# Optimization experiments

Measured on AMD Instinct MI355X. Metric: run time of the kernel, lower is better.

The kernel has to match this reference:

```python
import jax, jax.numpy as jnp
import numpy as np

B, H, P, D, NF = 16, 16, 128, 128, 12  # patches == head_dim required by lin_qk


def setup_inputs() -> dict:
    key = jax.random.key(0)
    ks = jax.random.split(key, 8)
    return {
        "q": jax.random.normal(ks[0], (B, H, P, D), jnp.float32),
        "k": jax.random.normal(ks[1], (B, H, P, D), jnp.float32),
        "scale": jnp.ones((1,), jnp.float32),  # unused by the original forward
        "grid": jnp.arange(NF, dtype=jnp.float32) + 1.0,
        "base_weight": jax.random.uniform(ks[2], (D, D), jnp.float32),
        "coef_q": jax.random.uniform(ks[3], (D, NF), jnp.float32),
        "coef_k": jax.random.uniform(ks[4], (D, NF), jnp.float32),
        "scale_base": jnp.ones((1, H, P, D), jnp.float32),
        "scale_sp": jnp.ones((1, H, P, D), jnp.float32),
        "w_qk": jax.random.normal(ks[5], (D, D), jnp.float32) / np.float32(np.sqrt(D)),
        "b_qk": jnp.zeros((D,), jnp.float32),
    }


def _branch(x, coef, grid, base_weight, scale_sp, scale_base):
    # base path: SiLU(x) @ W^T  (F.linear semantics)
    base = jax.nn.silu(x) @ base_weight.T
    # KAN sin basis: sin(grid_f * x_d) -> (B,H,P,NF,D); contract coef[d,f]
    s = jnp.sin(grid[:, None] * x[..., None, :])
    f = jnp.einsum('df,bhpfd->bhpd', coef, s)
    return jax.nn.sigmoid(f * scale_sp + base * scale_base)


def reference(q, k, scale, grid, base_weight, coef_q, coef_k, scale_base, scale_sp, w_qk, b_qk):
    # Per-channel sigmoids, then sum over D. The original builds the full
    # (B,H,P,P,D) broadcast tensor sig_q[...,p,None,:] + sig_k[...,None,p',:]
    # and sums over D; that is exactly separable:
    #   sum_d(sig_q[p,d]) + sum_d(sig_k[p',d])
    sq = _branch(q, coef_q, grid, base_weight, scale_sp, scale_base).sum(-1)  # (B,H,P)
    sk = _branch(k, coef_k, grid, base_weight, scale_sp, scale_base).sum(-1)  # (B,H,P)
    f_out = sq[..., :, None] + sk[..., None, :]  # (B,H,P,P)
    f_out = f_out @ w_qk.T + b_qk  # lin_qk: valid because patches == head_dim
    return jax.nn.softmax(f_out, axis=-1)
```

## Files before the change

kernel.cpp:

```cpp
#include <hip/hip_runtime.h>


typedef float          f32x4 __attribute__((ext_vector_type(4)));
typedef short          s16x8 __attribute__((ext_vector_type(8)));
typedef unsigned short u16x8 __attribute__((ext_vector_type(8)));
typedef unsigned short u16x4 __attribute__((ext_vector_type(4)));

static __device__ __forceinline__ unsigned short f2bf(float f) {
    unsigned int u = __float_as_uint(f);
    u += 0x7FFFu + ((u >> 16) & 1u);
    return (unsigned short)(u >> 16);
}
static __device__ __forceinline__ int swz(int local) {
    return local ^ (((local >> 8) & 7) << 4);
}

__global__ __launch_bounds__(256) void k_convert(const float* __restrict__ bw,
                                                 unsigned short* __restrict__ wbf) {
    int i = blockIdx.x * 256 + threadIdx.x;
    if (i < 128 * 128) wbf[i] = f2bf(bw[i]);
}

__global__ __launch_bounds__(512, 4) void k_branch(
    const float* __restrict__ q, const float* __restrict__ k,
    const unsigned short* __restrict__ wbf,
    const float* __restrict__ gridv,
    const float* __restrict__ coef_q, const float* __restrict__ coef_k,
    const float* __restrict__ sbase,
    const float* __restrict__ ssp,
    float* __restrict__ sums)
{
    __shared__ char smem[65536];
    float* F_l = (float*)smem;

    const int t = threadIdx.x;
    const int lane = t & 63, w = t >> 6;
    const int r15 = lane & 15, g4 = lane >> 4;
    const int c  = t & 31;
    const int rg = t >> 5;
    const int row0 = blockIdx.x * 128;
    const bool is_q = row0 < 32768;
    const float* X = is_q ? q : k;
    const float* coef = is_q ? coef_q : coef_k;
    const int xrow0 = is_q ? row0 : row0 - 32768;
    const float g1 = gridv[0];

    #pragma unroll
    for (int it = 0; it < 4; ++it) {
        int ci = it * 512 + t;
        u16x8 v = *(const u16x8*)&wbf[ci * 8];
        *(u16x8*)(smem + swz(ci * 16)) = v;
    }
    #pragma unroll
    for (int it = 0; it < 8; ++it) {
        int row = rg * 8 + it;
        float4 x4 = *(const float4*)&X[(xrow0 + row) * 128 + c * 4];
        float xv[4] = {x4.x, x4.y, x4.z, x4.w};
        u16x4 sv;
        #pragma unroll
        for (int j = 0; j < 4; ++j)
            sv[j] = f2bf(xv[j] / (1.f + __expf(-xv[j])));
        *(u16x4*)(smem + swz(32768 + row * 256 + c * 8)) = sv;
    }
    __syncthreads();

    f32x4 acc[8];
    #pragma unroll
    for (int n = 0; n < 8; ++n) acc[n] = (f32x4){0.f, 0.f, 0.f, 0.f};

    const int abase = 32768 + (w * 16 + r15) * 256 + g4 * 16;
    const int bbase = r15 * 256 + g4 * 16;
    #pragma unroll
    for (int s = 0; s < 4; ++s) {
        s16x8 af = *(const s16x8*)(smem + swz(abase + s * 64));
        #pragma unroll
        for (int n = 0; n < 8; ++n) {
            s16x8 bf = *(const s16x8*)(smem + swz(bbase + n * 4096 + s * 64));
            acc[n] = __builtin_amdgcn_mfma_f32_16x16x32_bf16(af, bf, acc[n], 0, 0, 0);
        }
    }
    __syncthreads();

    #pragma unroll
    for (int n = 0; n < 8; ++n) {
        int col = n * 16 + r15;
        #pragma unroll
        for (int reg = 0; reg < 4; ++reg) {
            int row = w * 16 + g4 * 4 + reg;
            F_l[row * 128 + col] = acc[n][reg];
        }
    }

    float cf[4][12];
    #pragma unroll
    for (int j = 0; j < 4; ++j) {
        const float4* cp = (const float4*)&coef[(c * 4 + j) * 12];
        float4 c0 = cp[0], c1 = cp[1], c2 = cp[2];
        cf[j][0] = c0.x; cf[j][1] = c0.y; cf[j][2]  = c0.z; cf[j][3]  = c0.w;
        cf[j][4] = c1.x; cf[j][5] = c1.y; cf[j][6]  = c1.z; cf[j][7]  = c1.w;
        cf[j][8] = c2.x; cf[j][9] = c2.y; cf[j][10] = c2.z; cf[j][11] = c2.w;
    }

    #pragma unroll
    for (int it = 0; it < 8; ++it) {
        int row = rg * 8 + it;
        int hp = (row0 + row) & 2047;
        float4 x4 = *(const float4*)&X[(xrow0 + row) * 128 + c * 4];
        f32x4 F4 = *(f32x4*)&F_l[row * 128 + c * 4];
        float4 sp = *(const float4*)&ssp[hp * 128 + c * 4];
        float4 sb = *(const float4*)&sbase[hp * 128 + c * 4];
        float xv[4] = {x4.x, x4.y, x4.z, x4.w};
        float spv[4] = {sp.x, sp.y, sp.z, sp.w};
        float sbv[4] = {sb.x, sb.y, sb.z, sb.w};
        float ps = 0.f;
        #pragma unroll
        for (int j = 0; j < 4; ++j) {
            float a = g1 * xv[j];
            float s1 = __sinf(a);
            float cv = __cosf(a);
            float t2 = cv + cv;
            float sprev = 0.f, scur = s1;
            float f = cf[j][0] * s1;
            #pragma unroll
            for (int u = 1; u < 12; ++u) {
                float snext = __builtin_fmaf(t2, scur, -sprev);
                f = __builtin_fmaf(cf[j][u], snext, f);
                sprev = scur; scur = snext;
            }
            float z = f * spv[j] + F4[j] * sbv[j];
            ps += 1.f / (1.f + __expf(-z));
        }
        ps += __shfl_xor(ps, 1, 64);
        ps += __shfl_xor(ps, 2, 64);
        ps += __shfl_xor(ps, 4, 64);
        ps += __shfl_xor(ps, 8, 64);
        ps += __shfl_xor(ps, 16, 64);
        if (c == 0) sums[row0 + row] = ps;
    }
}

__global__ __launch_bounds__(128) void k_tvec(
    const float* __restrict__ sums, const float* __restrict__ w_qk,
    const float* __restrict__ b_qk, float* __restrict__ T, float* __restrict__ R)
{
    __shared__ float skl[128];
    int bh = blockIdx.x;
    int t = threadIdx.x;
    const float4* wr = (const float4*)&w_qk[t * 128];
    if (bh < 256) {
        skl[t] = sums[32768 + bh * 128 + t];
        __syncthreads();
        float a = 0.f;
        #pragma unroll 8
        for (int p4 = 0; p4 < 32; ++p4) {
            float4 w4 = wr[p4];
            a += w4.x * skl[p4 * 4 + 0] + w4.y * skl[p4 * 4 + 1] +
                 w4.z * skl[p4 * 4 + 2] + w4.w * skl[p4 * 4 + 3];
        }
        T[bh * 128 + t] = a + b_qk[t];
    } else {
        float a = 0.f;
        #pragma unroll 8
        for (int p4 = 0; p4 < 32; ++p4) {
            float4 w4 = wr[p4];
            a += w4.x + w4.y + w4.z + w4.w;
        }
        R[t] = a;
    }
}

__global__ __launch_bounds__(256) void k_softmax(
    const float* __restrict__ sums, const float* __restrict__ T,
    const float* __restrict__ R, float* __restrict__ out)
{
    int row = blockIdx.x * 4 + (threadIdx.x >> 6);
    int lane = threadIdx.x & 63;
    int bh = row >> 7;
    float sqv = sums[row];
    float2 r2 = *(const float2*)&R[lane * 2];
    float2 t2 = *(const float2*)&T[bh * 128 + lane * 2];
    float l0 = sqv * r2.x + t2.x;
    float l1 = sqv * r2.y + t2.y;
    float m = fmaxf(l0, l1);
    #pragma unroll
    for (int s = 32; s >= 1; s >>= 1) m = fmaxf(m, __shfl_xor(m, s, 64));
    float e0 = __expf(l0 - m), e1 = __expf(l1 - m);
    float sum = e0 + e1;
    #pragma unroll
    for (int w2 = 32; w2 >= 1; w2 >>= 1) sum += __shfl_xor(sum, w2, 64);
    float inv = 1.f / sum;
    float2 o2 = {e0 * inv, e1 * inv};
    *(float2*)&out[row * 128 + lane * 2] = o2;
}

extern "C" void kernel_launch(void* const* d_in, const int* in_sizes, int n_in,
                              void* d_out, int out_size, void* d_ws, size_t ws_size,
                              hipStream_t stream) {
    (void)in_sizes; (void)n_in; (void)out_size; (void)ws_size;
    const float* q      = (const float*)d_in[0];
    const float* k      = (const float*)d_in[1];
    const float* gridv  = (const float*)d_in[3];
    const float* bw     = (const float*)d_in[4];
    const float* coef_q = (const float*)d_in[5];
    const float* coef_k = (const float*)d_in[6];
    const float* sbase  = (const float*)d_in[7];
    const float* ssp    = (const float*)d_in[8];
    const float* w_qk   = (const float*)d_in[9];
    const float* b_qk   = (const float*)d_in[10];

    float* out  = (float*)d_out;
    float* ws   = (float*)d_ws;
    float* sums = ws;
    float* R    = ws + 65536;
    float* T    = ws + 65664;
    unsigned short* wbf = (unsigned short*)(ws + 98432);

    k_convert<<<64, 256, 0, stream>>>(bw, wbf);
    k_branch<<<512, 512, 0, stream>>>(q, k, wbf, gridv, coef_q, coef_k,
                                      sbase, ssp, sums);
    k_tvec<<<257, 128, 0, stream>>>(sums, w_qk, b_qk, T, R);
    k_softmax<<<32768 / 4, 256, 0, stream>>>(sums, T, R, out);
}
```

Measured before the change: 46.68 us.

## Split branch kernel into separate sin-basis and bf16 MFMA GEMM kernels

Splits the fused branch kernel into two kernels. k_sin computes the scaled sin-basis contraction and writes it to a workspace buffer. k_gemm computes SiLU on the fly, reads the bf16 weights straight from global memory with no LDS staging, and uses a smaller skewed LDS tile per wave for the epilogue. The aim is higher occupancy and less LDS pressure in each kernel. The cost is an extra launch and a round trip of a 65536x128 fp32 intermediate (about 32MB write plus read) through memory.

```diff
diff --git a/kernel.cpp b/kernel.cpp
--- a/kernel.cpp
+++ b/kernel.cpp
@@ -4,15 +4,27 @@
 typedef float          f32x4 __attribute__((ext_vector_type(4)));
 typedef short          s16x8 __attribute__((ext_vector_type(8)));
 typedef unsigned short u16x8 __attribute__((ext_vector_type(8)));
-typedef unsigned short u16x4 __attribute__((ext_vector_type(4)));
 
 static __device__ __forceinline__ unsigned short f2bf(float f) {
     unsigned int u = __float_as_uint(f);
     u += 0x7FFFu + ((u >> 16) & 1u);
     return (unsigned short)(u >> 16);
 }
-static __device__ __forceinline__ int swz(int local) {
-    return local ^ (((local >> 8) & 7) << 4);
+
+static __device__ __forceinline__ float sindot12(float x, const float* cf, float g1) {
+    float a = g1 * x;
+    float s1 = __sinf(a);
+    float cv = __cosf(a);
+    float t2 = cv + cv;
+    float sprev = 0.f, scur = s1;
+    float f = cf[0] * s1;
+    #pragma unroll
+    for (int u = 1; u < 12; ++u) {
+        float sn = __builtin_fmaf(t2, scur, -sprev);
+        f = __builtin_fmaf(cf[u], sn, f);
+        sprev = scur; scur = sn;
+    }
+    return f;
 }
 
 __global__ __launch_bounds__(256) void k_convert(const float* __restrict__ bw,
@@ -21,113 +33,118 @@
     if (i < 128 * 128) wbf[i] = f2bf(bw[i]);
 }
 
-__global__ __launch_bounds__(512, 4) void k_branch(
+__global__ __launch_bounds__(256, 6) void k_sin(
     const float* __restrict__ q, const float* __restrict__ k,
-    const unsigned short* __restrict__ wbf,
     const float* __restrict__ gridv,
     const float* __restrict__ coef_q, const float* __restrict__ coef_k,
-    const float* __restrict__ sbase,
     const float* __restrict__ ssp,
-    float* __restrict__ sums)
-{
-    __shared__ char smem[65536];
-    float* F_l = (float*)smem;
-
+    float* __restrict__ fv)
+{
     const int t = threadIdx.x;
-    const int lane = t & 63, w = t >> 6;
-    const int r15 = lane & 15, g4 = lane >> 4;
-    const int c  = t & 31;
-    const int rg = t >> 5;
-    const int row0 = blockIdx.x * 128;
+    const int c2 = t & 63;
+    const int rg = t >> 6;
+    const int row0 = blockIdx.x * 64;
     const bool is_q = row0 < 32768;
     const float* X = is_q ? q : k;
     const float* coef = is_q ? coef_q : coef_k;
     const int xrow0 = is_q ? row0 : row0 - 32768;
     const float g1 = gridv[0];
 
-    #pragma unroll
-    for (int it = 0; it < 4; ++it) {
-        int ci = it * 512 + t;
-        u16x8 v = *(const u16x8*)&wbf[ci * 8];
-        *(u16x8*)(smem + swz(ci * 16)) = v;
-    }
-    #pragma unroll
-    for (int it = 0; it < 8; ++it) {
-        int row = rg * 8 + it;
-        float4 x4 = *(const float4*)&X[(xrow0 + row) * 128 + c * 4];
-        float xv[4] = {x4.x, x4.y, x4.z, x4.w};
-        u16x4 sv;
-        #pragma unroll
-        for (int j = 0; j < 4; ++j)
-            sv[j] = f2bf(xv[j] / (1.f + __expf(-xv[j])));
-        *(u16x4*)(smem + swz(32768 + row * 256 + c * 8)) = sv;
-    }
-    __syncthreads();
+    float cf0[12], cf1[12];
+    {
+        const float4* p0 = (const float4*)&coef[(c2 * 2) * 12];
+        float4 a0 = p0[0], a1 = p0[1], a2 = p0[2];
+        cf0[0]=a0.x; cf0[1]=a0.y; cf0[2]=a0.z; cf0[3]=a0.w;
+        cf0[4]=a1.x; cf0[5]=a1.y; cf0[6]=a1.z; cf0[7]=a1.w;
+        cf0[8]=a2.x; cf0[9]=a2.y; cf0[10]=a2.z; cf0[11]=a2.w;
+        const float4* p1 = (const float4*)&coef[(c2 * 2 + 1) * 12];
+        float4 b0 = p1[0], b1 = p1[1], b2 = p1[2];
+        cf1[0]=b0.x; cf1[1]=b0.y; cf1[2]=b0.z; cf1[3]=b0.w;
+        cf1[4]=b1.x; cf1[5]=b1.y; cf1[6]=b1.z; cf1[7]=b1.w;
+        cf1[8]=b2.x; cf1[9]=b2.y; cf1[10]=b2.z; cf1[11]=b2.w;
+    }
+
+    #pragma unroll
+    for (int i = 0; i < 16; ++i) {
+        int row = rg * 16 + i;
+        int grow = row0 + row;
+        int hp = grow & 2047;
+        float2 x2 = *(const float2*)&X[(xrow0 + row) * 128 + c2 * 2];
+        float2 sp = *(const float2*)&ssp[hp * 128 + c2 * 2];
+        float f0 = sindot12(x2.x, cf0, g1) * sp.x;
+        float f1 = sindot12(x2.y, cf1, g1) * sp.y;
+        float2 o = {f0, f1};
+        *(float2*)&fv[grow * 128 + c2 * 2] = o;
+    }
+}
+
+__global__ __launch_bounds__(256, 5) void k_gemm(
+    const float* __restrict__ q, const float* __restrict__ k,
+    const unsigned short* __restrict__ wbf,
+    const float* __restrict__ fv,
+    const float* __restrict__ sbase,
+    float* __restrict__ sums)
+{
+    __shared__ float F_l[4][2048];
+
+    const int t = threadIdx.x;
+    const int lane = t & 63, w = t >> 6;
+    const int r15 = lane & 15, g4 = lane >> 4;
+    const int row0 = blockIdx.x * 64;
+    const bool is_q = row0 < 32768;
+    const float* X = is_q ? q : k;
+    const int xrow0 = is_q ? row0 : row0 - 32768;
+
+    const float* xrowp = &X[(xrow0 + w * 16 + r15) * 128];
 
     f32x4 acc[8];
     #pragma unroll
     for (int n = 0; n < 8; ++n) acc[n] = (f32x4){0.f, 0.f, 0.f, 0.f};
 
-    const int abase = 32768 + (w * 16 + r15) * 256 + g4 * 16;
-    const int bbase = r15 * 256 + g4 * 16;
     #pragma unroll
     for (int s = 0; s < 4; ++s) {
-        s16x8 af = *(const s16x8*)(smem + swz(abase + s * 64));
+        const float4* xp = (const float4*)&xrowp[s * 32 + g4 * 8];
+        float4 x0 = xp[0], x1 = xp[1];
+        float xs[8] = {x0.x, x0.y, x0.z, x0.w, x1.x, x1.y, x1.z, x1.w};
+        s16x8 af;
+        #pragma unroll
+        for (int j = 0; j < 8; ++j) {
+            float s1 = xs[j] / (1.f + __expf(-xs[j]));
+            af[j] = (short)f2bf(s1);
+        }
         #pragma unroll
         for (int n = 0; n < 8; ++n) {
-            s16x8 bf = *(const s16x8*)(smem + swz(bbase + n * 4096 + s * 64));
+            s16x8 bf = *(const s16x8*)&wbf[(n * 16 + r15) * 128 + s * 32 + g4 * 8];
             acc[n] = __builtin_amdgcn_mfma_f32_16x16x32_bf16(af, bf, acc[n], 0, 0, 0);
         }
     }
-    __syncthreads();
 
     #pragma unroll
     for (int n = 0; n < 8; ++n) {
         int col = n * 16 + r15;
         #pragma unroll
         for (int reg = 0; reg < 4; ++reg) {
-            int row = w * 16 + g4 * 4 + reg;
-            F_l[row * 128 + col] = acc[n][reg];
-        }
-    }
-
-    float cf[4][12];
-    #pragma unroll
-    for (int j = 0; j < 4; ++j) {
-        const float4* cp = (const float4*)&coef[(c * 4 + j) * 12];
-        float4 c0 = cp[0], c1 = cp[1], c2 = cp[2];
-        cf[j][0] = c0.x; cf[j][1] = c0.y; cf[j][2]  = c0.z; cf[j][3]  = c0.w;
-        cf[j][4] = c1.x; cf[j][5] = c1.y; cf[j][6]  = c1.z; cf[j][7]  = c1.w;
-        cf[j][8] = c2.x; cf[j][9] = c2.y; cf[j][10] = c2.z; cf[j][11] = c2.w;
-    }
-
-    #pragma unroll
-    for (int it = 0; it < 8; ++it) {
-        int row = rg * 8 + it;
-        int hp = (row0 + row) & 2047;
-        float4 x4 = *(const float4*)&X[(xrow0 + row) * 128 + c * 4];
-        f32x4 F4 = *(f32x4*)&F_l[row * 128 + c * 4];
-        float4 sp = *(const float4*)&ssp[hp * 128 + c * 4];
-        float4 sb = *(const float4*)&sbase[hp * 128 + c * 4];
-        float xv[4] = {x4.x, x4.y, x4.z, x4.w};
-        float spv[4] = {sp.x, sp.y, sp.z, sp.w};
+            int rl = g4 * 4 + reg;
+            F_l[w][rl * 128 + ((col + rl * 4) & 127)] = acc[n][reg];
+        }
+    }
+
+    const int rr = lane >> 5;
+    const int c32 = lane & 31;
+    #pragma unroll
+    for (int i = 0; i < 8; ++i) {
+        int rl = rr * 8 + i;
+        int grow = row0 + w * 16 + rl;
+        int hp = grow & 2047;
+        f32x4 F4 = *(f32x4*)&F_l[w][rl * 128 + ((c32 * 4 + rl * 4) & 127)];
+        float4 fq = *(const float4*)&fv[grow * 128 + c32 * 4];
+        float4 sb = *(const float4*)&sbase[hp * 128 + c32 * 4];
+        float fvv[4] = {fq.x, fq.y, fq.z, fq.w};
         float sbv[4] = {sb.x, sb.y, sb.z, sb.w};
         float ps = 0.f;
         #pragma unroll
         for (int j = 0; j < 4; ++j) {
-            float a = g1 * xv[j];
-            float s1 = __sinf(a);
-            float cv = __cosf(a);
-            float t2 = cv + cv;
-            float sprev = 0.f, scur = s1;
-            float f = cf[j][0] * s1;
-            #pragma unroll
-            for (int u = 1; u < 12; ++u) {
-                float snext = __builtin_fmaf(t2, scur, -sprev);
-                f = __builtin_fmaf(cf[j][u], snext, f);
-                sprev = scur; scur = snext;
-            }
-            float z = f * spv[j] + F4[j] * sbv[j];
+            float z = fvv[j] + F4[j] * sbv[j];
             ps += 1.f / (1.f + __expf(-z));
         }
         ps += __shfl_xor(ps, 1, 64);
@@ -135,7 +152,7 @@
         ps += __shfl_xor(ps, 4, 64);
         ps += __shfl_xor(ps, 8, 64);
         ps += __shfl_xor(ps, 16, 64);
-        if (c == 0) sums[row0 + row] = ps;
+        if (c32 == 0) sums[grow] = ps;
     }
 }
 
@@ -214,10 +231,11 @@
     float* R    = ws + 65536;
     float* T    = ws + 65664;
     unsigned short* wbf = (unsigned short*)(ws + 98432);
+    float* fv   = ws + 106624;
 
     k_convert<<<64, 256, 0, stream>>>(bw, wbf);
-    k_branch<<<512, 512, 0, stream>>>(q, k, wbf, gridv, coef_q, coef_k,
-                                      sbase, ssp, sums);
+    k_sin<<<1024, 256, 0, stream>>>(q, k, gridv, coef_q, coef_k, ssp, fv);
+    k_gemm<<<1024, 256, 0, stream>>>(q, k, wbf, fv, sbase, sums);
     k_tvec<<<257, 128, 0, stream>>>(sums, w_qk, b_qk, T, R);
     k_softmax<<<32768 / 4, 256, 0, stream>>>(sums, T, R, out);
 }
```

Result: slower. 60.62 us (+29.9%).
